# Optimization experiments

Hardware: AMD Instinct MI355X
Metric: run time of the kernel (lower is better)

Reference implementation:

```python
import jax, jax.numpy as jnp
import numpy as np
import math

B, N, K, H = 2, 2048, 1024, 16
S = K // H  # head dim = 64


def apply_rope(t):
    # t: [b, h, N, s] -> rotary position embedding (rotate-half convention)
    s = t.shape[-1]
    pos = jnp.arange(t.shape[2], dtype=jnp.float32)
    inv_freq = 1.0 / (10000.0 ** (jnp.arange(0, s, 2, dtype=jnp.float32) / s))
    ang = pos[:, None] * inv_freq[None, :]               # [N, s/2]
    cos = jnp.concatenate([jnp.cos(ang), jnp.cos(ang)], axis=-1)  # [N, s]
    sin = jnp.concatenate([jnp.sin(ang), jnp.sin(ang)], axis=-1)
    t1, t2 = t[..., : s // 2], t[..., s // 2:]
    rot = jnp.concatenate([-t2, t1], axis=-1)
    return t * cos + rot * sin


def setup_inputs() -> dict:
    key = jax.random.key(0)
    ks = jax.random.split(key, 6)
    sc = 1.0 / math.sqrt(K)
    x = jax.random.normal(ks[0], (B, N, K), dtype=jnp.float32)
    Wq = jax.random.normal(ks[1], (K, K), dtype=jnp.float32) * sc
    Wk = jax.random.normal(ks[2], (K, K), dtype=jnp.float32) * sc
    Wv = jax.random.normal(ks[3], (K, K), dtype=jnp.float32) * sc
    Wu = jax.random.normal(ks[4], (K, K), dtype=jnp.float32) * sc
    bu = jax.random.normal(ks[5], (K,), dtype=jnp.float32) * 0.01
    mask = jnp.tril(jnp.ones((N, N), dtype=jnp.int32))  # causal
    return {"x": x, "Wq": Wq, "Wk": Wk, "Wv": Wv, "Wu": Wu, "bu": bu, "mask": mask}


def reference(x, Wq, Wk, Wv, Wu, bu, mask):
    b, n, k = x.shape
    h, s = H, S
    # torch Linear: y = x @ W.T
    def proj(W):
        return (x @ W.T).reshape(b, n, h, s).transpose(0, 2, 1, 3)  # [b,h,n,s]
    Q = apply_rope(proj(Wq))
    Kh = apply_rope(proj(Wk))
    V = proj(Wv)
    scores = jnp.einsum('bhqs,bhks->bhqk', Q, Kh) / math.sqrt(s)
    scores = jnp.where(mask[None, None, :, :] == 0, -jnp.inf, scores)
    attn = jax.nn.softmax(scores, axis=-1)
    out = jnp.einsum('bhqk,bhks->bhqs', attn, V)           # [b,h,n,s]
    out = out.transpose(0, 2, 1, 3).reshape(b, n, k)
    return out @ Wu.T + bu
```

## Files before the change

### kernel.cpp

```cpp
#include <hip/hip_runtime.h>
#include <hip/hip_bf16.h>

#define Bq 2
#define Nq 2048
#define Kq 1024
#define Hq 16
#define Sq 64
#define Mq (Bq * Nq)

typedef __attribute__((ext_vector_type(4))) float f32x4;
typedef __attribute__((ext_vector_type(8))) short bf16x8;

__device__ unsigned short g_xb[(size_t)Mq * Kq];
__device__ unsigned short g_Wqb[Kq * Kq];
__device__ unsigned short g_Wkb[Kq * Kq];
__device__ unsigned short g_Wvb[Kq * Kq];
__device__ unsigned short g_Wub[Kq * Kq];
__device__ unsigned short g_Qb[(size_t)Bq * Hq * Nq * Sq];
__device__ unsigned short g_Kb[(size_t)Bq * Hq * Nq * Sq];
__device__ unsigned short g_Vb[(size_t)Bq * Hq * Nq * Sq];
__device__ unsigned short g_Vt[(size_t)Bq * Hq * Sq * Nq];
__device__ unsigned short g_Ao[(size_t)Mq * Kq];

__device__ __forceinline__ unsigned short f2bf(float f) {
    union { float f; unsigned int i; } u; u.f = f;
    unsigned int r = u.i + 0x7FFF + ((u.i >> 16) & 1);
    return (unsigned short)(r >> 16);
}
__device__ __forceinline__ float bf2f(unsigned short u) {
    union { unsigned int i; float f; } v; v.i = ((unsigned int)u) << 16;
    return v.f;
}
__device__ __forceinline__ void async16(const unsigned short* g, unsigned short* l) {
    __builtin_amdgcn_global_load_lds(
        (const __attribute__((address_space(1))) void*)g,
        (__attribute__((address_space(3))) void*)l, 16, 0, 0);
}

__global__ __launch_bounds__(256) void convert_all_kernel(
    const float* __restrict__ x,  const float* __restrict__ wq,
    const float* __restrict__ wk, const float* __restrict__ wv,
    const float* __restrict__ wu)
{
    int i = blockIdx.x * 256 + threadIdx.x;
    const float* src; unsigned short* dst; int off;
    if (i < 1048576) { src = x; dst = g_xb; off = i; }
    else {
        int j = i - 1048576;
        int which = j >> 18;
        off = j & 262143;
        src = (which == 0) ? wq : (which == 1) ? wk : (which == 2) ? wv : wu;
        dst = (which == 0) ? g_Wqb : (which == 1) ? g_Wkb : (which == 2) ? g_Wvb : g_Wub;
    }
    float4 v = ((const float4*)src)[off];
    ushort4 o;
    o.x = f2bf(v.x); o.y = f2bf(v.y); o.z = f2bf(v.z); o.w = f2bf(v.w);
    ((ushort4*)dst)[off] = o;
}

__global__ __launch_bounds__(256) void qkv_gemm_kernel()
{
    __shared__ __align__(16) unsigned short As[2][128][64];
    __shared__ __align__(16) unsigned short Bs[2][128][64];

    const int n0 = blockIdx.x * 128;
    const int m0 = blockIdx.y * 128;
    const int which = n0 >> 10;
    const unsigned short* A  = g_xb;
    const unsigned short* Bm = (which == 0) ? g_Wqb : (which == 1) ? g_Wkb : g_Wvb;
    unsigned short* dst      = (which == 0) ? g_Qb : (which == 1) ? g_Kb : g_Vb;
    const int nb = n0 & 1023;

    const int tid = threadIdx.x;
    const int w = tid >> 6, l = tid & 63;
    const int lane16 = l & 15, quad = l >> 4;
    const int wm = (w >> 1) * 64, wn = (w & 1) * 64;

    const int sr = l >> 3;
    const int sc = ((l & 7) ^ sr) * 8;
    const int rsw = (lane16 & 7);

    f32x4 acc[4][4];
#pragma unroll
    for (int mi = 0; mi < 4; ++mi)
#pragma unroll
        for (int ni = 0; ni < 4; ++ni) acc[mi][ni] = (f32x4){0.f, 0.f, 0.f, 0.f};

#pragma unroll
    for (int c = 0; c < 4; ++c) {
        async16(A  + (size_t)(m0 + 32 * w + 8 * c + sr) * Kq + sc, &As[0][32 * w + 8 * c][0]);
        async16(Bm + (size_t)(nb + 32 * w + 8 * c + sr) * Kq + sc, &Bs[0][32 * w + 8 * c][0]);
    }
    __syncthreads();

    int cur = 0;
    for (int kt = 0; kt < Kq; kt += 64) {
        if (kt + 64 < Kq) {
            int nxt = cur ^ 1;
#pragma unroll
            for (int c = 0; c < 4; ++c) {
                async16(A  + (size_t)(m0 + 32 * w + 8 * c + sr) * Kq + kt + 64 + sc, &As[nxt][32 * w + 8 * c][0]);
                async16(Bm + (size_t)(nb + 32 * w + 8 * c + sr) * Kq + kt + 64 + sc, &Bs[nxt][32 * w + 8 * c][0]);
            }
        }
#pragma unroll
        for (int ks = 0; ks < 2; ++ks) {
            bf16x8 af[4], bfr[4];
#pragma unroll
            for (int mi = 0; mi < 4; ++mi)
                af[mi]  = *(const bf16x8*)&As[cur][wm + mi * 16 + lane16][((ks * 4 + quad) ^ rsw) * 8];
#pragma unroll
            for (int ni = 0; ni < 4; ++ni)
                bfr[ni] = *(const bf16x8*)&Bs[cur][wn + ni * 16 + lane16][((ks * 4 + quad) ^ rsw) * 8];
#pragma unroll
            for (int mi = 0; mi < 4; ++mi)
#pragma unroll
                for (int ni = 0; ni < 4; ++ni)
                    acc[mi][ni] = __builtin_amdgcn_mfma_f32_16x16x32_bf16(af[mi], bfr[ni], acc[mi][ni], 0, 0, 0);
        }
        __syncthreads();
        cur ^= 1;
    }

#pragma unroll
    for (int mi = 0; mi < 4; ++mi)
#pragma unroll
        for (int ni = 0; ni < 4; ++ni)
#pragma unroll
            for (int r = 0; r < 4; ++r) {
                int m = m0 + wm + mi * 16 + quad * 4 + r;
                int n = n0 + wn + ni * 16 + lane16;
                unsigned short v = f2bf(acc[mi][ni][r]);
                int b = m >> 11, nn = m & 2047;
                int o = n & 1023, h = o >> 6, s = o & 63;
                dst[(((size_t)b * Hq + h) * Nq + nn) * Sq + s] = v;
            }
}

__global__ __launch_bounds__(256) void rope_vtrans_kernel()
{
    __shared__ unsigned short T[64][72];

    if (blockIdx.y < 2) {
        unsigned short* buf = (blockIdx.y == 0) ? g_Qb : g_Kb;
        const int idx = blockIdx.x * 256 + threadIdx.x;
        const int i  = idx & 31;
        const int n  = (idx >> 5) & (Nq - 1);
        const int bh = idx >> 16;
        const size_t base = ((size_t)bh * Nq + n) * Sq + i;

        float t1 = bf2f(buf[base]);
        float t2 = bf2f(buf[base + 32]);
        float inv_freq = exp2f((float)i * -0.41524101f);
        float ang = (float)n * inv_freq;
        float sn = __sinf(ang), cs = __cosf(ang);
        buf[base]      = f2bf(t1 * cs - t2 * sn);
        buf[base + 32] = f2bf(t2 * cs + t1 * sn);
    } else {
        if (blockIdx.x >= 1024) return;
        const int n0 = (blockIdx.x & 31) * 64;
        const int bh = blockIdx.x >> 5;
        const unsigned short* src = g_Vb + (size_t)bh * Nq * Sq;
        unsigned short* dst       = g_Vt + (size_t)bh * Sq * Nq;
        const int tid = threadIdx.x;
        const int r = tid >> 3, c8 = (tid & 7) * 8;

        uint4 a0 = *(const uint4*)(src + (size_t)(n0 + r) * Sq + c8);
        uint4 a1 = *(const uint4*)(src + (size_t)(n0 + r + 32) * Sq + c8);
        *(uint4*)&T[r][c8] = a0;
        *(uint4*)&T[r + 32][c8] = a1;
        __syncthreads();

        union { ushort4 u4[2]; unsigned short u[8]; } p0, p1;
#pragma unroll
        for (int j = 0; j < 8; ++j) { p0.u[j] = T[c8 + j][r]; p1.u[j] = T[c8 + j][r + 32]; }
        *(uint4*)(dst + (size_t)r * Nq + n0 + c8)        = *(uint4*)&p0;
        *(uint4*)(dst + (size_t)(r + 32) * Nq + n0 + c8) = *(uint4*)&p1;
    }
}

__global__ __launch_bounds__(512) void attn_kernel()
{
    const int bh = blockIdx.x;
    const int j  = blockIdx.y;
    const int qt = (j < 8) ? (15 - j) : (j - 8);
    const int q0 = qt * 128;
    const unsigned short* Qp = g_Qb + (size_t)bh * Nq * Sq;
    const unsigned short* Kp = g_Kb + (size_t)bh * Nq * Sq;
    const unsigned short* Vp = g_Vt + (size_t)bh * Sq * Nq;

    __shared__ __align__(16) unsigned short Ks[3][64][64];
    __shared__ __align__(16) unsigned short Vs[3][64][64];
    __shared__ __align__(16) unsigned short Ps[128][64];
    unsigned short* psf = &Ps[0][0];

    const int tid = threadIdx.x;
    const int w = tid >> 6, l = tid & 63;
    const int lane16 = l & 15, quad = l >> 4;
    const int sr = l >> 3;
    const int sc = ((l & 7) ^ sr) * 8;
    const int rsw = (lane16 & 7);

    bf16x8 be;
    {
        short o = (lane16 == 0) ? (short)0x3F80 : (short)0;
#pragma unroll
        for (int i = 0; i < 8; ++i) be[i] = o;
    }

    const int qlo = q0 + 16 * w;
    bf16x8 aq0 = *(const bf16x8*)(Qp + (size_t)(qlo + lane16) * Sq + quad * 8);
    bf16x8 aq1 = *(const bf16x8*)(Qp + (size_t)(qlo + lane16) * Sq + quad * 8 + 32);
    asm volatile("" : "+v"(aq0), "+v"(aq1));

    f32x4 Oacc[4];
    f32x4 Oext = (f32x4){0.f, 0.f, 0.f, 0.f};
#pragma unroll
    for (int ds = 0; ds < 4; ++ds) Oacc[ds] = (f32x4){0.f, 0.f, 0.f, 0.f};

    const float C1 = 0.18033688f;
    const float C2 = 11.54156036f;

    const int ntiles = 2 * qt + 2;

#define STAGE(t, b)                                                           \
    do {                                                                      \
        int kn_ = (t) * 64;                                                   \
        async16(Kp + (size_t)(kn_ + 8 * w + sr) * Sq + sc, &Ks[(b)][8 * w][0]);\
        async16(Vp + (size_t)(8 * w + sr) * Nq + kn_ + sc, &Vs[(b)][8 * w][0]);\
    } while (0)

    STAGE(0, 0);
    STAGE(1, 1);
    asm volatile("s_waitcnt vmcnt(2)" ::: "memory");
    __builtin_amdgcn_s_barrier();
    __builtin_amdgcn_sched_barrier(0);

    int cur = 0;
    for (int kb = 0; kb < ntiles; ++kb) {
        if (kb + 2 < ntiles) STAGE(kb + 2, (kb + 2) % 3);

        if (kb * 64 <= qlo + 15) {
            f32x4 S[4];
#pragma unroll
            for (int kc = 0; kc < 4; ++kc) S[kc] = (f32x4){0.f, 0.f, 0.f, 0.f};
#pragma unroll
            for (int kc = 0; kc < 4; ++kc) {
                const unsigned short* krow = &Ks[cur][kc * 16 + lane16][0];
                bf16x8 bk0 = *(const bf16x8*)&krow[(quad ^ rsw) * 8];
                bf16x8 bk1 = *(const bf16x8*)&krow[((4 + quad) ^ rsw) * 8];
                S[kc] = __builtin_amdgcn_mfma_f32_16x16x32_bf16(aq0, bk0, S[kc], 0, 0, 0);
                S[kc] = __builtin_amdgcn_mfma_f32_16x16x32_bf16(aq1, bk1, S[kc], 0, 0, 0);
            }

            const int qbase = qlo + quad * 4;
            if (kb * 64 + 63 > qlo) {
#pragma unroll
                for (int kc = 0; kc < 4; ++kc) {
                    int kpos = kb * 64 + kc * 16 + lane16;
#pragma unroll
                    for (int r = 0; r < 4; ++r)
                        S[kc][r] = (kpos <= qbase + r) ? exp2f(fmaf(S[kc][r], C1, -C2)) : 0.0f;
                }
            } else {
#pragma unroll
                for (int kc = 0; kc < 4; ++kc)
#pragma unroll
                    for (int r = 0; r < 4; ++r)
                        S[kc][r] = exp2f(fmaf(S[kc][r], C1, -C2));
            }

#pragma unroll
            for (int kc = 0; kc < 4; ++kc)
#pragma unroll
                for (int r = 0; r < 4; ++r) {
                    int prow = 16 * w + quad * 4 + r;
                    psf[(prow * 64 + kc * 16 + lane16) ^ ((prow & 7) << 3)] =
                        (unsigned short)(__float_as_uint(S[kc][r]) >> 16);
                }

            const int prow2 = 16 * w + lane16;
#pragma unroll
            for (int kk = 0; kk < 2; ++kk) {
                bf16x8 pa = *(const bf16x8*)(psf +
                    ((prow2 * 64 + kk * 32 + quad * 8) ^ (rsw << 3)));
#pragma unroll
                for (int ds = 0; ds < 4; ++ds) {
                    bf16x8 vb = *(const bf16x8*)&Vs[cur][ds * 16 + lane16][((kk * 4 + quad) ^ rsw) * 8];
                    Oacc[ds] = __builtin_amdgcn_mfma_f32_16x16x32_bf16(pa, vb, Oacc[ds], 0, 0, 0);
                }
                Oext = __builtin_amdgcn_mfma_f32_16x16x32_bf16(pa, be, Oext, 0, 0, 0);
            }
        }

        __builtin_amdgcn_sched_barrier(0);
        if (kb + 2 < ntiles) {
            asm volatile("s_waitcnt vmcnt(2)" ::: "memory");
        } else {
            asm volatile("s_waitcnt vmcnt(0)" ::: "memory");
        }
        __builtin_amdgcn_s_barrier();
        __builtin_amdgcn_sched_barrier(0);
        cur = (cur == 2) ? 0 : cur + 1;
    }
#undef STAGE

    const int b = bh >> 4, h = bh & 15;
    float inv[4];
#pragma unroll
    for (int r = 0; r < 4; ++r) {
        float lr = __shfl(Oext[r], quad * 16, 64);
        inv[r] = 1.0f / lr;
    }
#pragma unroll
    for (int ds = 0; ds < 4; ++ds)
#pragma unroll
        for (int r = 0; r < 4; ++r) {
            int nn = qlo + quad * 4 + r;
            g_Ao[((size_t)b * Nq + nn) * Kq + h * Sq + ds * 16 + lane16] =
                f2bf(Oacc[ds][r] * inv[r]);
        }
}

__global__ __launch_bounds__(256) void out_gemm_kernel(
    const float* __restrict__ bu, float* __restrict__ out)
{
    __shared__ __align__(16) unsigned short As[2][128][64];
    __shared__ __align__(16) unsigned short Bs[2][128][64];

    const int n0 = blockIdx.x * 128;
    const int m0 = blockIdx.y * 128;

    const int tid = threadIdx.x;
    const int w = tid >> 6, l = tid & 63;
    const int lane16 = l & 15, quad = l >> 4;
    const int wm = (w >> 1) * 64, wn = (w & 1) * 64;
    const int sr = l >> 3;
    const int sc = ((l & 7) ^ sr) * 8;
    const int rsw = (lane16 & 7);

    f32x4 acc[4][4];
#pragma unroll
    for (int mi = 0; mi < 4; ++mi)
#pragma unroll
        for (int ni = 0; ni < 4; ++ni) acc[mi][ni] = (f32x4){0.f, 0.f, 0.f, 0.f};

#pragma unroll
    for (int c = 0; c < 4; ++c) {
        async16(g_Ao  + (size_t)(m0 + 32 * w + 8 * c + sr) * Kq + sc, &As[0][32 * w + 8 * c][0]);
        async16(g_Wub + (size_t)(n0 + 32 * w + 8 * c + sr) * Kq + sc, &Bs[0][32 * w + 8 * c][0]);
    }
    __syncthreads();

    int cur = 0;
    for (int kt = 0; kt < Kq; kt += 64) {
        if (kt + 64 < Kq) {
            int nxt = cur ^ 1;
#pragma unroll
            for (int c = 0; c < 4; ++c) {
                async16(g_Ao  + (size_t)(m0 + 32 * w + 8 * c + sr) * Kq + kt + 64 + sc, &As[nxt][32 * w + 8 * c][0]);
                async16(g_Wub + (size_t)(n0 + 32 * w + 8 * c + sr) * Kq + kt + 64 + sc, &Bs[nxt][32 * w + 8 * c][0]);
            }
        }
#pragma unroll
        for (int ks = 0; ks < 2; ++ks) {
            bf16x8 af[4], bfr[4];
#pragma unroll
            for (int mi = 0; mi < 4; ++mi)
                af[mi]  = *(const bf16x8*)&As[cur][wm + mi * 16 + lane16][((ks * 4 + quad) ^ rsw) * 8];
#pragma unroll
            for (int ni = 0; ni < 4; ++ni)
                bfr[ni] = *(const bf16x8*)&Bs[cur][wn + ni * 16 + lane16][((ks * 4 + quad) ^ rsw) * 8];
#pragma unroll
            for (int mi = 0; mi < 4; ++mi)
#pragma unroll
                for (int ni = 0; ni < 4; ++ni)
                    acc[mi][ni] = __builtin_amdgcn_mfma_f32_16x16x32_bf16(af[mi], bfr[ni], acc[mi][ni], 0, 0, 0);
        }
        __syncthreads();
        cur ^= 1;
    }

#pragma unroll
    for (int mi = 0; mi < 4; ++mi)
#pragma unroll
        for (int ni = 0; ni < 4; ++ni)
#pragma unroll
            for (int r = 0; r < 4; ++r) {
                int m = m0 + wm + mi * 16 + quad * 4 + r;
                int n = n0 + wn + ni * 16 + lane16;
                out[(size_t)m * Kq + n] = acc[mi][ni][r] + bu[n];
            }
}

extern "C" void kernel_launch(void* const* d_in, const int* in_sizes, int n_in,
                              void* d_out, int out_size, void* d_ws, size_t ws_size,
                              hipStream_t stream)
{
    const float* x  = (const float*)d_in[0];
    const float* Wq = (const float*)d_in[1];
    const float* Wk = (const float*)d_in[2];
    const float* Wv = (const float*)d_in[3];
    const float* Wu = (const float*)d_in[4];
    const float* bu = (const float*)d_in[5];
    float* out = (float*)d_out;

    convert_all_kernel<<<8192, 256, 0, stream>>>(x, Wq, Wk, Wv, Wu);
    qkv_gemm_kernel<<<dim3(24, 32), 256, 0, stream>>>();
    rope_vtrans_kernel<<<dim3(8192, 3), 256, 0, stream>>>();
    attn_kernel<<<dim3(32, 16), 512, 0, stream>>>();
    out_gemm_kernel<<<dim3(8, 32), 256, 0, stream>>>(bu, out);
}
```

Measured before the change: 221.6 us.

## Fuse RoPE and V transpose into QKV GEMM, split long attention tiles across blocks

The QKV GEMM now applies RoPE to Q/K in its epilogue and writes V transposed through LDS, so the separate rope/transpose kernel and the g_Vb round trip go away. The GEMM main loop also moves from double-buffered 64-wide K steps to a triple-buffered 32-wide pipeline with explicit waitcnt and barriers. Attention splits the longer causal query tiles into 2 or 3 key-range chunks, using constant tables, to balance work across 30×32 blocks. Partial unnormalized outputs and row sums are written in fp32 and merged by a new combine kernel, which adds extra global traffic and a launch in exchange for better load balance.

Result: no change. 224.8 us (+1.4%).

```diff
diff --git a/kernel.cpp b/kernel.cpp
--- a/kernel.cpp
+++ b/kernel.cpp
@@ -18,9 +18,16 @@
 __device__ unsigned short g_Wub[Kq * Kq];
 __device__ unsigned short g_Qb[(size_t)Bq * Hq * Nq * Sq];
 __device__ unsigned short g_Kb[(size_t)Bq * Hq * Nq * Sq];
-__device__ unsigned short g_Vb[(size_t)Bq * Hq * Nq * Sq];
 __device__ unsigned short g_Vt[(size_t)Bq * Hq * Sq * Nq];
 __device__ unsigned short g_Ao[(size_t)Mq * Kq];
+__device__ __align__(16) float g_On[(size_t)32 * 16 * 3 * 128 * 64];
+__device__ float g_Ol[32 * 16 * 3 * 128];
+
+__constant__ signed char c_qt[30] = {15,15,15,14,14,14,13,13,13,12,12,12,11,11,10,10,9,9,8,8,7,7,6,6,5,4,3,2,1,0};
+__constant__ signed char c_t0[30] = {0,11,22,0,10,20,0,10,19,0,9,18,0,12,0,11,0,10,0,9,0,8,0,7,0,0,0,0,0,0};
+__constant__ signed char c_t1[30] = {11,22,32,10,20,30,10,19,28,9,18,26,12,24,11,22,10,20,9,18,8,16,7,14,12,10,8,6,4,2};
+__constant__ signed char c_sp[30] = {0,1,2,0,1,2,0,1,2,0,1,2,0,1,0,1,0,1,0,1,0,1,0,1,0,0,0,0,0,0};
+__constant__ signed char c_ns[30] = {3,3,3,3,3,3,3,3,3,3,3,3,2,2,2,2,2,2,2,2,2,2,2,2,1,1,1,1,1,1};
 
 __device__ __forceinline__ unsigned short f2bf(float f) {
     union { float f; unsigned int i; } u; u.f = f;
@@ -60,15 +67,16 @@
 
 __global__ __launch_bounds__(256) void qkv_gemm_kernel()
 {
-    __shared__ __align__(16) unsigned short As[2][128][64];
-    __shared__ __align__(16) unsigned short Bs[2][128][64];
+    __shared__ __align__(16) unsigned short SLDS[24576];
+    auto As = (unsigned short (*)[128][32])(SLDS);
+    auto Bs = (unsigned short (*)[128][32])(SLDS + 12288);
 
     const int n0 = blockIdx.x * 128;
     const int m0 = blockIdx.y * 128;
     const int which = n0 >> 10;
     const unsigned short* A  = g_xb;
     const unsigned short* Bm = (which == 0) ? g_Wqb : (which == 1) ? g_Wkb : g_Wvb;
-    unsigned short* dst      = (which == 0) ? g_Qb : (which == 1) ? g_Kb : g_Vb;
+    unsigned short* dst      = (which == 0) ? g_Qb : g_Kb;
     const int nb = n0 & 1023;
 
     const int tid = threadIdx.x;
@@ -76,9 +84,9 @@
     const int lane16 = l & 15, quad = l >> 4;
     const int wm = (w >> 1) * 64, wn = (w & 1) * 64;
 
-    const int sr = l >> 3;
-    const int sc = ((l & 7) ^ sr) * 8;
-    const int rsw = (lane16 & 7);
+    const int sr  = l >> 2;
+    const int sc  = ((l & 3) ^ ((l >> 3) & 3)) * 8;
+    const int rsw = (lane16 >> 1) & 3;
 
     f32x4 acc[4][4];
 #pragma unroll
@@ -86,104 +94,112 @@
 #pragma unroll
         for (int ni = 0; ni < 4; ++ni) acc[mi][ni] = (f32x4){0.f, 0.f, 0.f, 0.f};
 
-#pragma unroll
-    for (int c = 0; c < 4; ++c) {
-        async16(A  + (size_t)(m0 + 32 * w + 8 * c + sr) * Kq + sc, &As[0][32 * w + 8 * c][0]);
-        async16(Bm + (size_t)(nb + 32 * w + 8 * c + sr) * Kq + sc, &Bs[0][32 * w + 8 * c][0]);
-    }
-    __syncthreads();
+#define QSTAGE(t, b)                                                            \
+    do {                                                                        \
+        _Pragma("unroll")                                                       \
+        for (int c = 0; c < 2; ++c) {                                           \
+            async16(A  + (size_t)(m0 + 32 * w + 16 * c + sr) * Kq + (t) * 32 + sc, \
+                    &As[(b)][32 * w + 16 * c][0]);                              \
+            async16(Bm + (size_t)(nb + 32 * w + 16 * c + sr) * Kq + (t) * 32 + sc, \
+                    &Bs[(b)][32 * w + 16 * c][0]);                              \
+        }                                                                       \
+    } while (0)
+
+    QSTAGE(0, 0);
+    QSTAGE(1, 1);
+    asm volatile("s_waitcnt vmcnt(4)" ::: "memory");
+    __builtin_amdgcn_s_barrier();
+    __builtin_amdgcn_sched_barrier(0);
 
     int cur = 0;
-    for (int kt = 0; kt < Kq; kt += 64) {
-        if (kt + 64 < Kq) {
-            int nxt = cur ^ 1;
-#pragma unroll
-            for (int c = 0; c < 4; ++c) {
-                async16(A  + (size_t)(m0 + 32 * w + 8 * c + sr) * Kq + kt + 64 + sc, &As[nxt][32 * w + 8 * c][0]);
-                async16(Bm + (size_t)(nb + 32 * w + 8 * c + sr) * Kq + kt + 64 + sc, &Bs[nxt][32 * w + 8 * c][0]);
-            }
-        }
-#pragma unroll
-        for (int ks = 0; ks < 2; ++ks) {
-            bf16x8 af[4], bfr[4];
-#pragma unroll
-            for (int mi = 0; mi < 4; ++mi)
-                af[mi]  = *(const bf16x8*)&As[cur][wm + mi * 16 + lane16][((ks * 4 + quad) ^ rsw) * 8];
+    for (int kb = 0; kb < 32; ++kb) {
+        if (kb + 2 < 32) QSTAGE(kb + 2, (kb + 2) % 3);
+
+        bf16x8 af[4], bfr[4];
+#pragma unroll
+        for (int mi = 0; mi < 4; ++mi)
+            af[mi]  = *(const bf16x8*)&As[cur][wm + mi * 16 + lane16][(quad ^ rsw) * 8];
+#pragma unroll
+        for (int ni = 0; ni < 4; ++ni)
+            bfr[ni] = *(const bf16x8*)&Bs[cur][wn + ni * 16 + lane16][(quad ^ rsw) * 8];
+#pragma unroll
+        for (int mi = 0; mi < 4; ++mi)
 #pragma unroll
             for (int ni = 0; ni < 4; ++ni)
-                bfr[ni] = *(const bf16x8*)&Bs[cur][wn + ni * 16 + lane16][((ks * 4 + quad) ^ rsw) * 8];
-#pragma unroll
-            for (int mi = 0; mi < 4; ++mi)
-#pragma unroll
-                for (int ni = 0; ni < 4; ++ni)
-                    acc[mi][ni] = __builtin_amdgcn_mfma_f32_16x16x32_bf16(af[mi], bfr[ni], acc[mi][ni], 0, 0, 0);
-        }
-        __syncthreads();
-        cur ^= 1;
-    }
-
-#pragma unroll
-    for (int mi = 0; mi < 4; ++mi)
-#pragma unroll
-        for (int ni = 0; ni < 4; ++ni)
+                acc[mi][ni] = __builtin_amdgcn_mfma_f32_16x16x32_bf16(af[mi], bfr[ni], acc[mi][ni], 0, 0, 0);
+
+        __builtin_amdgcn_sched_barrier(0);
+        if (kb + 2 < 32) {
+            asm volatile("s_waitcnt vmcnt(4)" ::: "memory");
+        } else {
+            asm volatile("s_waitcnt vmcnt(0)" ::: "memory");
+        }
+        __builtin_amdgcn_s_barrier();
+        __builtin_amdgcn_sched_barrier(0);
+        cur = (cur == 2) ? 0 : cur + 1;
+    }
+#undef QSTAGE
+
+    const int h0 = (n0 & 1023) >> 6;
+    if (which < 2) {
+        const float invf0 = exp2f((float)lane16 * -0.41524101f);
+        const float invf1 = exp2f((float)(lane16 + 16) * -0.41524101f);
+        const int h = h0 + (wn >> 6);
+#pragma unroll
+        for (int mi = 0; mi < 4; ++mi)
 #pragma unroll
             for (int r = 0; r < 4; ++r) {
                 int m = m0 + wm + mi * 16 + quad * 4 + r;
-                int n = n0 + wn + ni * 16 + lane16;
-                unsigned short v = f2bf(acc[mi][ni][r]);
                 int b = m >> 11, nn = m & 2047;
-                int o = n & 1023, h = o >> 6, s = o & 63;
-                dst[(((size_t)b * Hq + h) * Nq + nn) * Sq + s] = v;
-            }
-}
-
-__global__ __launch_bounds__(256) void rope_vtrans_kernel()
-{
-    __shared__ unsigned short T[64][72];
-
-    if (blockIdx.y < 2) {
-        unsigned short* buf = (blockIdx.y == 0) ? g_Qb : g_Kb;
-        const int idx = blockIdx.x * 256 + threadIdx.x;
-        const int i  = idx & 31;
-        const int n  = (idx >> 5) & (Nq - 1);
-        const int bh = idx >> 16;
-        const size_t base = ((size_t)bh * Nq + n) * Sq + i;
-
-        float t1 = bf2f(buf[base]);
-        float t2 = bf2f(buf[base + 32]);
-        float inv_freq = exp2f((float)i * -0.41524101f);
-        float ang = (float)n * inv_freq;
-        float sn = __sinf(ang), cs = __cosf(ang);
-        buf[base]      = f2bf(t1 * cs - t2 * sn);
-        buf[base + 32] = f2bf(t2 * cs + t1 * sn);
+                float np = (float)nn;
+                float a0 = np * invf0, a1 = np * invf1;
+                float s0 = __sinf(a0), c0 = __cosf(a0);
+                float s1 = __sinf(a1), c1 = __cosf(a1);
+                float t10 = acc[mi][0][r], t20 = acc[mi][2][r];
+                float t11 = acc[mi][1][r], t21 = acc[mi][3][r];
+                unsigned short* dr = dst + (((size_t)b * Hq + h) * Nq + nn) * Sq + lane16;
+                dr[0]  = f2bf(t10 * c0 - t20 * s0);
+                dr[16] = f2bf(t11 * c1 - t21 * s1);
+                dr[32] = f2bf(t20 * c0 + t10 * s0);
+                dr[48] = f2bf(t21 * c1 + t11 * s1);
+            }
     } else {
-        if (blockIdx.x >= 1024) return;
-        const int n0 = (blockIdx.x & 31) * 64;
-        const int bh = blockIdx.x >> 5;
-        const unsigned short* src = g_Vb + (size_t)bh * Nq * Sq;
-        unsigned short* dst       = g_Vt + (size_t)bh * Sq * Nq;
-        const int tid = threadIdx.x;
-        const int r = tid >> 3, c8 = (tid & 7) * 8;
-
-        uint4 a0 = *(const uint4*)(src + (size_t)(n0 + r) * Sq + c8);
-        uint4 a1 = *(const uint4*)(src + (size_t)(n0 + r + 32) * Sq + c8);
-        *(uint4*)&T[r][c8] = a0;
-        *(uint4*)&T[r + 32][c8] = a1;
+        unsigned short* T = SLDS;
+#pragma unroll
+        for (int mi = 0; mi < 4; ++mi)
+#pragma unroll
+            for (int ni = 0; ni < 4; ++ni)
+#pragma unroll
+                for (int r = 0; r < 4; ++r) {
+                    int nl = wn + ni * 16 + lane16;
+                    int ml = wm + mi * 16 + quad * 4 + r;
+                    T[nl * 136 + ml] = f2bf(acc[mi][ni][r]);
+                }
         __syncthreads();
-
-        union { ushort4 u4[2]; unsigned short u[8]; } p0, p1;
-#pragma unroll
-        for (int j = 0; j < 8; ++j) { p0.u[j] = T[c8 + j][r]; p1.u[j] = T[c8 + j][r + 32]; }
-        *(uint4*)(dst + (size_t)r * Nq + n0 + c8)        = *(uint4*)&p0;
-        *(uint4*)(dst + (size_t)(r + 32) * Nq + n0 + c8) = *(uint4*)&p1;
+        const int b = m0 >> 11, mcol = m0 & 2047;
+#pragma unroll
+        for (int rr = 0; rr < 4; ++rr) {
+            int row = rr * 32 + (tid >> 3);
+            int h = h0 + (row >> 6), s = row & 63;
+            unsigned short* drow = g_Vt + (((size_t)b * Hq + h) * Sq + s) * Nq + mcol;
+#pragma unroll
+            for (int ci = 0; ci < 2; ++ci) {
+                int c = ci * 8 + (tid & 7);
+                *(uint4*)(drow + c * 8) = *(const uint4*)(T + row * 136 + c * 8);
+            }
+        }
     }
 }
 
 __global__ __launch_bounds__(512) void attn_kernel()
 {
     const int bh = blockIdx.x;
-    const int j  = blockIdx.y;
-    const int qt = (j < 8) ? (15 - j) : (j - 8);
+    const int y  = blockIdx.y;
+    const int qt  = c_qt[y];
+    const int t0  = c_t0[y];
+    const int t1  = c_t1[y];
+    const int sp  = c_sp[y];
+    const int nsp = c_ns[y];
     const int q0 = qt * 128;
     const unsigned short* Qp = g_Qb + (size_t)bh * Nq * Sq;
     const unsigned short* Kp = g_Kb + (size_t)bh * Nq * Sq;
@@ -221,8 +237,6 @@
     const float C1 = 0.18033688f;
     const float C2 = 11.54156036f;
 
-    const int ntiles = 2 * qt + 2;
-
 #define STAGE(t, b)                                                           \
     do {                                                                      \
         int kn_ = (t) * 64;                                                   \
@@ -230,15 +244,15 @@
         async16(Vp + (size_t)(8 * w + sr) * Nq + kn_ + sc, &Vs[(b)][8 * w][0]);\
     } while (0)
 
-    STAGE(0, 0);
-    STAGE(1, 1);
+    STAGE(t0, 0);
+    STAGE(t0 + 1, 1);
     asm volatile("s_waitcnt vmcnt(2)" ::: "memory");
     __builtin_amdgcn_s_barrier();
     __builtin_amdgcn_sched_barrier(0);
 
     int cur = 0;
-    for (int kb = 0; kb < ntiles; ++kb) {
-        if (kb + 2 < ntiles) STAGE(kb + 2, (kb + 2) % 3);
+    for (int kb = t0; kb < t1; ++kb) {
+        if (kb + 2 < t1) STAGE(kb + 2, (kb - t0 + 2) % 3);
 
         if (kb * 64 <= qlo + 15) {
             f32x4 S[4];
@@ -294,7 +308,7 @@
         }
 
         __builtin_amdgcn_sched_barrier(0);
-        if (kb + 2 < ntiles) {
+        if (kb + 2 < t1) {
             asm volatile("s_waitcnt vmcnt(2)" ::: "memory");
         } else {
             asm volatile("s_waitcnt vmcnt(0)" ::: "memory");
@@ -305,21 +319,70 @@
     }
 #undef STAGE
 
-    const int b = bh >> 4, h = bh & 15;
-    float inv[4];
-#pragma unroll
-    for (int r = 0; r < 4; ++r) {
-        float lr = __shfl(Oext[r], quad * 16, 64);
-        inv[r] = 1.0f / lr;
-    }
-#pragma unroll
-    for (int ds = 0; ds < 4; ++ds)
+    if (nsp == 1) {
+        const int b = bh >> 4, h = bh & 15;
+        float inv[4];
 #pragma unroll
         for (int r = 0; r < 4; ++r) {
-            int nn = qlo + quad * 4 + r;
-            g_Ao[((size_t)b * Nq + nn) * Kq + h * Sq + ds * 16 + lane16] =
-                f2bf(Oacc[ds][r] * inv[r]);
-        }
+            float lr = __shfl(Oext[r], quad * 16, 64);
+            inv[r] = 1.0f / lr;
+        }
+#pragma unroll
+        for (int ds = 0; ds < 4; ++ds)
+#pragma unroll
+            for (int r = 0; r < 4; ++r) {
+                int nn = qlo + quad * 4 + r;
+                g_Ao[((size_t)b * Nq + nn) * Kq + h * Sq + ds * 16 + lane16] =
+                    f2bf(Oacc[ds][r] * inv[r]);
+            }
+    } else {
+        float* On = g_On + (((size_t)bh * 16 + qt) * 3 + sp) * (128 * 64);
+        float* Ol = g_Ol + (((size_t)bh * 16 + qt) * 3 + sp) * 128;
+#pragma unroll
+        for (int r = 0; r < 4; ++r) {
+            float lr = __shfl(Oext[r], quad * 16, 64);
+            if (lane16 == 0) Ol[16 * w + quad * 4 + r] = lr;
+        }
+#pragma unroll
+        for (int ds = 0; ds < 4; ++ds)
+#pragma unroll
+            for (int r = 0; r < 4; ++r)
+                On[(16 * w + quad * 4 + r) * 64 + ds * 16 + lane16] = Oacc[ds][r];
+    }
+}
+
+__global__ __launch_bounds__(256) void attn_combine_kernel()
+{
+    const int bh = blockIdx.x;
+    const int qt = 6 + blockIdx.y;
+    const int nsp = (qt >= 12) ? 3 : 2;
+    const int tid = threadIdx.x;
+    const int row = tid >> 1;
+    const int ch  = (tid & 1) * 32;
+    const size_t sb = ((size_t)bh * 16 + qt) * 3;
+    const float* On0 = g_On + (sb + 0) * (128 * 64);
+    const float* On1 = g_On + (sb + 1) * (128 * 64);
+    const float* On2 = g_On + (sb + 2) * (128 * 64);
+    const float* Ol  = g_Ol + sb * 128;
+
+    float lsum = Ol[row] + Ol[128 + row];
+    if (nsp == 3) lsum += Ol[256 + row];
+    float inv = 1.0f / lsum;
+
+    const int b = bh >> 4, h = bh & 15, nn = qt * 128 + row;
+    unsigned short* dst = g_Ao + ((size_t)b * Nq + nn) * Kq + h * Sq + ch;
+
+#pragma unroll
+    for (int j = 0; j < 8; ++j) {
+        int o = row * 64 + ch + j * 4;
+        f32x4 v = *(const f32x4*)(On0 + o);
+        v += *(const f32x4*)(On1 + o);
+        if (nsp == 3) v += *(const f32x4*)(On2 + o);
+        ushort4 u;
+        u.x = f2bf(v[0] * inv); u.y = f2bf(v[1] * inv);
+        u.z = f2bf(v[2] * inv); u.w = f2bf(v[3] * inv);
+        ((ushort4*)dst)[j] = u;
+    }
 }
 
 __global__ __launch_bounds__(256) void out_gemm_kernel(
@@ -407,7 +470,7 @@
 
     convert_all_kernel<<<8192, 256, 0, stream>>>(x, Wq, Wk, Wv, Wu);
     qkv_gemm_kernel<<<dim3(24, 32), 256, 0, stream>>>();
-    rope_vtrans_kernel<<<dim3(8192, 3), 256, 0, stream>>>();
-    attn_kernel<<<dim3(32, 16), 512, 0, stream>>>();
+    attn_kernel<<<dim3(32, 30), 512, 0, stream>>>();
+    attn_combine_kernel<<<dim3(32, 10), 256, 0, stream>>>();
     out_gemm_kernel<<<dim3(8, 32), 256, 0, stream>>>(bu, out);
 }
```
